# Kernel tuning notes

Hardware: AMD Instinct MI355X
Metric: run time of the kernel (lower is better)

## Reference

```python
import jax, jax.numpy as jnp
import numpy as np

N = 50000      # nodes
E = 800000     # edges
D_IN = 128
HID = 128
L = 3          # local_layers
EPS = 1e-5     # LayerNorm eps


def setup_inputs() -> dict:
    key = jax.random.key(0)
    ks = jax.random.split(key, 8)
    s_in = 1.0 / np.sqrt(D_IN)
    s_h = 1.0 / np.sqrt(HID)
    return {
        "x": jax.random.normal(ks[0], (N, D_IN), jnp.float32),
        "edge_index": jax.random.randint(ks[1], (2, E), 0, N, dtype=jnp.int64),
        "lin_in_w": jax.random.normal(ks[2], (D_IN, HID), jnp.float32) * s_in,
        "lin_in_b": jnp.zeros((HID,), jnp.float32),
        "conv_w": jax.random.normal(ks[3], (L, HID, HID), jnp.float32) * s_h,
        "conv_b": jnp.zeros((L, HID), jnp.float32),
        "lin_w": jax.random.normal(ks[4], (L, HID, HID), jnp.float32) * s_h,
        "lin_b": jnp.zeros((L, HID), jnp.float32),
        "ln_g": jnp.ones((L, HID), jnp.float32),
        "ln_b": jnp.zeros((L, HID), jnp.float32),
    }


def reference(x, edge_index, lin_in_w, lin_in_b, conv_w, conv_b, lin_w, lin_b, ln_g, ln_b):
    # GCNConv(normalize=True, add_self_loops=True): augment with self loops
    loops = jnp.arange(N, dtype=edge_index.dtype)
    src = jnp.concatenate([edge_index[0], loops])
    dst = jnp.concatenate([edge_index[1], loops])
    deg = jax.ops.segment_sum(jnp.ones_like(dst, x.dtype), dst, num_segments=N)
    dinv = jnp.where(deg > 0, jax.lax.rsqrt(deg), 0.0)
    norm = dinv[src] * dinv[dst]  # [E+N]

    # pre_linear (dropout p=0, eval)
    x = x @ lin_in_w + lin_in_b

    x_final = jnp.zeros((N, HID), x.dtype)
    for i in range(L):
        h = x @ conv_w[i]
        agg = jax.ops.segment_sum(h[src] * norm[:, None], dst, num_segments=N) + conv_b[i]
        # residual linear
        x = agg + x @ lin_w[i] + lin_b[i]
        # LayerNorm
        mu = jnp.mean(x, axis=-1, keepdims=True)
        var = jnp.var(x, axis=-1, keepdims=True)
        x = (x - mu) * jax.lax.rsqrt(var + EPS) * ln_g[i] + ln_b[i]
        x = jax.nn.relu(x)
        x_final = x_final + x  # JK sum
    return x_final
```

## Files before the change

kernel.cpp:

```cpp
#include <hip/hip_runtime.h>

#define HID 128
#define LN_EPS 1e-5f

typedef __attribute__((ext_vector_type(8))) short bf16x8;
typedef __attribute__((ext_vector_type(4))) float f32x4;

__device__ __forceinline__ ushort f2bf(float v) {
  union { float f; uint u; } x; x.f = v;
  uint r = x.u + 0x7fffu + ((x.u >> 16) & 1u);
  return (ushort)(r >> 16);
}
__device__ __forceinline__ float bf2f(ushort u) {
  union { uint u; float f; } x; x.u = (uint)u << 16; return x.f;
}


__global__ void k_init(int* __restrict__ cnt, int n) {
  int i = blockIdx.x * 256 + threadIdx.x;
  if (i < n) cnt[i] = 0;
}

__global__ void k_count(const int* __restrict__ dst, int* __restrict__ cnt,
                        int* __restrict__ rank, int E) {
  int e = blockIdx.x * 256 + threadIdx.x;
  if (e < E) rank[e] = atomicAdd(&cnt[dst[e]], 1);
}

__global__ void k_dinv(const int* __restrict__ cnt, float* __restrict__ dinv, int n) {
  int i = blockIdx.x * 256 + threadIdx.x;
  if (i < n) dinv[i] = rsqrtf((float)cnt[i] + 1.0f);
}

__global__ void k_bsum(const int* __restrict__ cnt, int* __restrict__ bsum, int n) {
  __shared__ int red[256];
  int b = blockIdx.x, t = threadIdx.x;
  int i = b * 512 + t * 2;
  int s = ((i < n) ? cnt[i] : 0) + ((i + 1 < n) ? cnt[i + 1] : 0);
  red[t] = s;
  __syncthreads();
  for (int off = 128; off > 0; off >>= 1) {
    if (t < off) red[t] += red[t + off];
    __syncthreads();
  }
  if (t == 0) bsum[b] = red[0];
}

__global__ void k_bscan(int* __restrict__ bsum, int nb) {
  __shared__ int buf[1024];
  int t = threadIdx.x;
  int v = (t < nb) ? bsum[t] : 0;
  buf[t] = v;
  __syncthreads();
  for (int off = 1; off < 1024; off <<= 1) {
    int u = (t >= off) ? buf[t - off] : 0;
    __syncthreads();
    buf[t] += u;
    __syncthreads();
  }
  if (t < nb) bsum[t] = buf[t] - v;
}

__global__ void k_rowstart(const int* __restrict__ cnt, const int* __restrict__ bsum,
                           int* __restrict__ row_start, int n) {
  __shared__ int buf[256];
  int b = blockIdx.x, t = threadIdx.x;
  int i = b * 512 + t * 2;
  int c0 = (i < n) ? cnt[i] : 0;
  int c1 = (i + 1 < n) ? cnt[i + 1] : 0;
  int s = c0 + c1;
  buf[t] = s;
  __syncthreads();
  int mine = s;
  for (int off = 1; off < 256; off <<= 1) {
    int u = (t >= off) ? buf[t - off] : 0;
    __syncthreads();
    buf[t] += u;
    __syncthreads();
  }
  int ex = buf[t] - mine + bsum[b];
  if (i < n) row_start[i] = ex;
  if (i + 1 < n) row_start[i + 1] = ex + c0;
}

__global__ void k_scatter(const int* __restrict__ src, const int* __restrict__ dst,
                          const int* __restrict__ row_start, const int* __restrict__ rank,
                          const float* __restrict__ dinv,
                          uint2* __restrict__ rec, int E) {
  int e = blockIdx.x * 256 + threadIdx.x;
  if (e < E) {
    int d = dst[e], s = src[e];
    int pos = row_start[d] + rank[e];
    union { float f; uint u; } w; w.f = dinv[s] * dinv[d];
    rec[pos] = make_uint2((uint)s, w.u);
  }
}

__global__ void k_prep_w(const float* __restrict__ lin_in_w,
                         const float* __restrict__ conv_w, const float* __restrict__ lin_w,
                         const float* __restrict__ conv_b, const float* __restrict__ lin_b,
                         ushort* __restrict__ wt_in, ushort* __restrict__ wt_l,
                         float* __restrict__ bsum, int L) {
  int tid = blockIdx.x * 256 + threadIdx.x;
  int total = L * 128 * 256;
  if (tid < total) {
    int l = tid >> 15;
    int idx = tid & 32767;
    int n = idx >> 12;
    int r = idx & 4095;
    int ks = r >> 9;
    int r2 = r & 511;
    int lane = r2 >> 3;
    int j = r2 & 7;
    int k2 = ks * 32 + (lane >> 4) * 8 + j;
    int c = n * 16 + (lane & 15);
    float v = (k2 < 128) ? conv_w[((size_t)l * 128 + k2) * 128 + c]
                         : lin_w[((size_t)l * 128 + (k2 - 128)) * 128 + c];
    wt_l[tid] = f2bf(v);
  }
  if (tid < 128 * 128) {
    int n = tid >> 11;
    int r = tid & 2047;
    int ks = r >> 9;
    int r2 = r & 511;
    int lane = r2 >> 3;
    int j = r2 & 7;
    int k = ks * 32 + (lane >> 4) * 8 + j;
    int c = n * 16 + (lane & 15);
    wt_in[tid] = f2bf(lin_in_w[k * 128 + c]);
  }
  if (tid < L * 128) bsum[tid] = conv_b[tid] + lin_b[tid];
}

__global__ void k_agg(const ushort* __restrict__ X, const int* __restrict__ row_start,
                      const int* __restrict__ cnt, const float* __restrict__ dinv,
                      const uint2* __restrict__ rec, ushort* __restrict__ Sout, int n) {
  int node = blockIdx.x * 4 + (threadIdx.x >> 6);
  if (node >= n) return;
  int lane = threadIdx.x & 63;
  float dv = dinv[node];
  uint v = *reinterpret_cast<const uint*>(X + (size_t)node * HID + lane * 2);
  float ax = dv * dv * bf2f((ushort)(v & 0xffff));
  float ay = dv * dv * bf2f((ushort)(v >> 16));
  int start = row_start[node];
  int m = cnt[node];
  int last = start + m - 1;
  const ulong* recq = reinterpret_cast<const ulong*>(rec);

  for (int e = 0; e < m; e += 8) {
    int i0 = start + e;
    ulong q[8];
#pragma unroll
    for (int j = 0; j < 8; j++) q[j] = recq[min(i0 + j, last)];
    uint u[8];
#pragma unroll
    for (int j = 0; j < 8; j++)
      u[j] = *reinterpret_cast<const uint*>(X + (size_t)(uint)q[j] * HID + lane * 2);
#pragma unroll
    for (int j = 0; j < 8; j++) {
      union { uint u; float f; } w;
      w.u = (e + j < m) ? (uint)(q[j] >> 32) : 0u;
      ax = fmaf(w.f, bf2f((ushort)(u[j] & 0xffff)), ax);
      ay = fmaf(w.f, bf2f((ushort)(u[j] >> 16)), ay);
    }
  }
  uint o = (uint)f2bf(ax) | ((uint)f2bf(ay) << 16);
  *reinterpret_cast<uint*>(Sout + (size_t)node * HID + lane * 2) = o;
}


__global__ void __launch_bounds__(256, 2)
k_gemm_in(const float* __restrict__ Xin, const ushort* __restrict__ WtF,
          const float* __restrict__ bias, ushort* __restrict__ Xout, int nrows) {
  __shared__ float lds[4 * 16 * 132];
  const int tid = threadIdx.x;
  const int wid = tid >> 6, lane = tid & 63;
  const int lr = lane & 15, lg = lane >> 4;
  const int r0 = blockIdx.x * 64 + wid * 16;
  const int arow = r0 + lr;
  const bool rowok = arow < nrows;

  bf16x8 a[4];
  {
    const float* xp = Xin + (size_t)arow * HID + lg * 8;
#pragma unroll
    for (int ks = 0; ks < 4; ks++) {
      bf16x8 t;
#pragma unroll
      for (int i = 0; i < 8; i++) t[i] = 0;
      if (rowok) {
        float4 u0 = *reinterpret_cast<const float4*>(xp + ks * 32);
        float4 u1 = *reinterpret_cast<const float4*>(xp + ks * 32 + 4);
        t[0] = (short)f2bf(u0.x); t[1] = (short)f2bf(u0.y);
        t[2] = (short)f2bf(u0.z); t[3] = (short)f2bf(u0.w);
        t[4] = (short)f2bf(u1.x); t[5] = (short)f2bf(u1.y);
        t[6] = (short)f2bf(u1.z); t[7] = (short)f2bf(u1.w);
      }
      a[ks] = t;
    }
  }

  f32x4 acc[8];
#pragma unroll
  for (int n = 0; n < 8; n++) acc[n] = f32x4{0.f, 0.f, 0.f, 0.f};

  const ushort* wb = WtF + lane * 8;
#pragma unroll
  for (int n = 0; n < 8; n++)
#pragma unroll
    for (int ks = 0; ks < 4; ks++) {
      bf16x8 b = *reinterpret_cast<const bf16x8*>(wb + (n * 4 + ks) * 512);
      acc[n] = __builtin_amdgcn_mfma_f32_16x16x32_bf16(a[ks], b, acc[n], 0, 0, 0);
    }

  float* T = lds + wid * (16 * 132);
#pragma unroll
  for (int n = 0; n < 8; n++)
#pragma unroll
    for (int q = 0; q < 4; q++)
      T[(lg * 4 + q) * 132 + n * 16 + lr] = acc[n][q];

  const int c0 = lg * 32;
  const float* Trow = T + lr * 132 + c0;
  const int orow = r0 + lr;
  if (orow < nrows) {
    ushort* xo = Xout + (size_t)orow * HID + c0;
    uint pk[16];
#pragma unroll
    for (int j = 0; j < 8; j++) {
      float4 t = *reinterpret_cast<const float4*>(Trow + j * 4);
      float4 b4 = *reinterpret_cast<const float4*>(bias + c0 + j * 4);
      float o0 = t.x + b4.x, o1 = t.y + b4.y, o2 = t.z + b4.z, o3 = t.w + b4.w;
      pk[j * 2 + 0] = (uint)f2bf(o0) | ((uint)f2bf(o1) << 16);
      pk[j * 2 + 1] = (uint)f2bf(o2) | ((uint)f2bf(o3) << 16);
    }
#pragma unroll
    for (int j = 0; j < 4; j++)
      *reinterpret_cast<uint4*>(xo + j * 8) =
          make_uint4(pk[j * 4 + 0], pk[j * 4 + 1], pk[j * 4 + 2], pk[j * 4 + 3]);
  }
}

__global__ void __launch_bounds__(256, 2)
k_layer(const ushort* __restrict__ S, const ushort* __restrict__ Xin,
        ushort* __restrict__ Xout,
        const ushort* __restrict__ WtF, const float* __restrict__ bsum,
        const float* __restrict__ gamma, const float* __restrict__ beta, int nrows) {
  __shared__ float lds[4 * 16 * 132];
  const int tid = threadIdx.x;
  const int wid = tid >> 6, lane = tid & 63;
  const int lr = lane & 15, lg = lane >> 4;
  const int r0 = blockIdx.x * 64 + wid * 16;
  const int arow = r0 + lr;
  const bool rowok = arow < nrows;

  bf16x8 a[8];
  {
    const ushort* sp = S + (size_t)arow * HID + lg * 8;
    const ushort* xp = Xin + (size_t)arow * HID + lg * 8;
    bf16x8 z;
#pragma unroll
    for (int i = 0; i < 8; i++) z[i] = 0;
#pragma unroll
    for (int ks = 0; ks < 4; ks++)
      a[ks] = rowok ? *reinterpret_cast<const bf16x8*>(sp + ks * 32) : z;
#pragma unroll
    for (int ks = 0; ks < 4; ks++)
      a[4 + ks] = rowok ? *reinterpret_cast<const bf16x8*>(xp + ks * 32) : z;
  }

  f32x4 acc[8];
#pragma unroll
  for (int n = 0; n < 8; n++) acc[n] = f32x4{0.f, 0.f, 0.f, 0.f};

  const ushort* wb = WtF + lane * 8;
#pragma unroll
  for (int n = 0; n < 8; n++)
#pragma unroll
    for (int ks = 0; ks < 8; ks++) {
      bf16x8 b = *reinterpret_cast<const bf16x8*>(wb + (n * 8 + ks) * 512);
      acc[n] = __builtin_amdgcn_mfma_f32_16x16x32_bf16(a[ks], b, acc[n], 0, 0, 0);
    }

  float* T = lds + wid * (16 * 132);
#pragma unroll
  for (int n = 0; n < 8; n++)
#pragma unroll
    for (int q = 0; q < 4; q++)
      T[(lg * 4 + q) * 132 + n * 16 + lr] = acc[n][q];

  const int c0 = lg * 32;
  const float* Trow = T + lr * 132 + c0;
  float v[32];
  float sum = 0.f, sq = 0.f;
#pragma unroll
  for (int j = 0; j < 8; j++) {
    float4 t = *reinterpret_cast<const float4*>(Trow + j * 4);
    float4 b4 = *reinterpret_cast<const float4*>(bsum + c0 + j * 4);
    float x0 = t.x + b4.x, x1 = t.y + b4.y, x2 = t.z + b4.z, x3 = t.w + b4.w;
    v[j * 4 + 0] = x0; v[j * 4 + 1] = x1; v[j * 4 + 2] = x2; v[j * 4 + 3] = x3;
    sum += (x0 + x1) + (x2 + x3);
    sq = fmaf(x0, x0, sq); sq = fmaf(x1, x1, sq);
    sq = fmaf(x2, x2, sq); sq = fmaf(x3, x3, sq);
  }
  sum += __shfl_xor(sum, 16); sq += __shfl_xor(sq, 16);
  sum += __shfl_xor(sum, 32); sq += __shfl_xor(sq, 32);
  const float mean = sum * (1.f / 128.f);
  const float rstd = rsqrtf(sq * (1.f / 128.f) - mean * mean + LN_EPS);

  const int orow = r0 + lr;
  if (orow < nrows) {
    ushort* xo = Xout + (size_t)orow * HID + c0;
    uint pk[16];
#pragma unroll
    for (int j = 0; j < 8; j++) {
      float4 g4 = *reinterpret_cast<const float4*>(gamma + c0 + j * 4);
      float4 b4 = *reinterpret_cast<const float4*>(beta + c0 + j * 4);
      float o0 = fmaxf(fmaf((v[j * 4 + 0] - mean) * rstd, g4.x, b4.x), 0.f);
      float o1 = fmaxf(fmaf((v[j * 4 + 1] - mean) * rstd, g4.y, b4.y), 0.f);
      float o2 = fmaxf(fmaf((v[j * 4 + 2] - mean) * rstd, g4.z, b4.z), 0.f);
      float o3 = fmaxf(fmaf((v[j * 4 + 3] - mean) * rstd, g4.w, b4.w), 0.f);
      pk[j * 2 + 0] = (uint)f2bf(o0) | ((uint)f2bf(o1) << 16);
      pk[j * 2 + 1] = (uint)f2bf(o2) | ((uint)f2bf(o3) << 16);
    }
#pragma unroll
    for (int j = 0; j < 4; j++)
      *reinterpret_cast<uint4*>(xo + j * 8) =
          make_uint4(pk[j * 4 + 0], pk[j * 4 + 1], pk[j * 4 + 2], pk[j * 4 + 3]);
  }
}

__global__ void k_jk(const ushort* __restrict__ a, const ushort* __restrict__ b,
                     const ushort* __restrict__ c, float* __restrict__ out, int total8) {
  int i = blockIdx.x * 256 + threadIdx.x;
  if (i >= total8) return;
  uint4 ua = *reinterpret_cast<const uint4*>(a + (size_t)i * 8);
  uint4 ub = *reinterpret_cast<const uint4*>(b + (size_t)i * 8);
  uint4 uc = *reinterpret_cast<const uint4*>(c + (size_t)i * 8);
  float o[8];
  const uint pa[4] = {ua.x, ua.y, ua.z, ua.w};
  const uint pb[4] = {ub.x, ub.y, ub.z, ub.w};
  const uint pc[4] = {uc.x, uc.y, uc.z, uc.w};
#pragma unroll
  for (int j = 0; j < 4; j++) {
    o[j * 2 + 0] = bf2f((ushort)(pa[j] & 0xffff)) + bf2f((ushort)(pb[j] & 0xffff)) +
                   bf2f((ushort)(pc[j] & 0xffff));
    o[j * 2 + 1] = bf2f((ushort)(pa[j] >> 16)) + bf2f((ushort)(pb[j] >> 16)) +
                   bf2f((ushort)(pc[j] >> 16));
  }
  float* op = out + (size_t)i * 8;
  *reinterpret_cast<float4*>(op) = make_float4(o[0], o[1], o[2], o[3]);
  *reinterpret_cast<float4*>(op + 4) = make_float4(o[4], o[5], o[6], o[7]);
}


extern "C" void kernel_launch(void* const* d_in, const int* in_sizes, int n_in,
                              void* d_out, int out_size, void* d_ws, size_t ws_size,
                              hipStream_t stream) {
  const float* x_in     = (const float*)d_in[0];
  const int*   edge     = (const int*)d_in[1];
  const float* lin_in_w = (const float*)d_in[2];
  const float* lin_in_b = (const float*)d_in[3];
  const float* conv_w   = (const float*)d_in[4];
  const float* conv_b   = (const float*)d_in[5];
  const float* lin_w    = (const float*)d_in[6];
  const float* lin_b    = (const float*)d_in[7];
  const float* ln_g     = (const float*)d_in[8];
  const float* ln_b     = (const float*)d_in[9];

  int N = in_sizes[0] / HID;
  int E = in_sizes[1] / 2;
  int L = in_sizes[4] / (HID * HID);

  const int* src = edge;
  const int* dst = edge + E;

  char* ws = (char*)d_ws;
  size_t off = 0;
  auto alloc = [&](size_t bytes) -> void* {
    void* p = (void*)(ws + off);
    off += (bytes + 255) & ~(size_t)255;
    return p;
  };
  int*    cnt       = (int*)alloc((size_t)N * 4);
  int*    rank      = (int*)alloc((size_t)E * 4);
  int*    row_start = (int*)alloc((size_t)N * 4);
  float*  dinv      = (float*)alloc((size_t)N * 4);
  int*    blocksum  = (int*)alloc(4096);
  uint2*  rec       = (uint2*)alloc((size_t)E * 8);
  ushort* xb0       = (ushort*)alloc((size_t)N * HID * 2);
  ushort* xb1       = (ushort*)alloc((size_t)N * HID * 2);
  ushort* xb2       = (ushort*)alloc((size_t)N * HID * 2);
  ushort* sbuf      = (ushort*)alloc((size_t)N * HID * 2);
  ushort* wt_in     = (ushort*)alloc((size_t)128 * 128 * 2);
  ushort* wt_l      = (ushort*)alloc((size_t)L * 128 * 256 * 2);
  float*  bsum      = (float*)alloc((size_t)L * 128 * 4);
  (void)ws_size; (void)n_in; (void)out_size;

  int nb_n = (N + 255) / 256;
  int nb_e = (E + 255) / 256;
  int nbs  = (N + 511) / 512;
  int nb_g = (N + 63) / 64;
  int nb_w = (L * 128 * 256 + 255) / 256;
  int total8 = N * HID / 8;
  int nb_j = (total8 + 255) / 256;

  k_init<<<nb_n, 256, 0, stream>>>(cnt, N);
  k_count<<<nb_e, 256, 0, stream>>>(dst, cnt, rank, E);
  k_dinv<<<nb_n, 256, 0, stream>>>(cnt, dinv, N);
  k_bsum<<<nbs, 256, 0, stream>>>(cnt, blocksum, N);
  k_bscan<<<1, 1024, 0, stream>>>(blocksum, nbs);
  k_rowstart<<<nbs, 256, 0, stream>>>(cnt, blocksum, row_start, N);
  k_scatter<<<nb_e, 256, 0, stream>>>(src, dst, row_start, rank, dinv, rec, E);
  k_prep_w<<<nb_w, 256, 0, stream>>>(lin_in_w, conv_w, lin_w, conv_b, lin_b,
                                     wt_in, wt_l, bsum, L);

  k_gemm_in<<<nb_g, 256, 0, stream>>>(x_in, wt_in, lin_in_b, xb0, N);

  ushort* xin_b[3]  = {xb0, xb1, xb2};
  ushort* xout_b[3] = {xb1, xb2, xb0};
  for (int i = 0; i < L; i++) {
    k_agg<<<(N + 3) / 4, 256, 0, stream>>>(xin_b[i], row_start, cnt, dinv, rec, sbuf, N);
    k_layer<<<nb_g, 256, 0, stream>>>(sbuf, xin_b[i], xout_b[i],
        wt_l + (size_t)i * 128 * 256, bsum + (size_t)i * 128,
        ln_g + (size_t)i * HID, ln_b + (size_t)i * HID, N);
  }
  k_jk<<<nb_j, 256, 0, stream>>>(xb1, xb2, xb0, (float*)d_out, total8);
}
```

Baseline: 361.2 us.

## Split aggregation into column halves, stage weights in LDS, fuse JK sum and dinv

The dinv computation moves into the block-sum kernel, and the JK summation moves into the last layer kernel. Both changes remove a separate launch, and the JK fusion also skips one full write and read of a bf16 buffer. The aggregation kernel now runs in two passes over 64-column halves, with each wave handling two edges at once and combining them through a cross-lane shuffle. This aims to improve gather locality and cache reuse of node rows, at the cost of reading the edge records twice. The layer GEMM now stages weight tiles through LDS with double-buffered prefetch instead of loading per-lane from global memory, which adds syncs and LDS use that may reduce occupancy.

```diff
diff --git a/kernel.cpp b/kernel.cpp
--- a/kernel.cpp
+++ b/kernel.cpp
@@ -27,17 +27,16 @@
   if (e < E) rank[e] = atomicAdd(&cnt[dst[e]], 1);
 }
 
-__global__ void k_dinv(const int* __restrict__ cnt, float* __restrict__ dinv, int n) {
-  int i = blockIdx.x * 256 + threadIdx.x;
-  if (i < n) dinv[i] = rsqrtf((float)cnt[i] + 1.0f);
-}
-
-__global__ void k_bsum(const int* __restrict__ cnt, int* __restrict__ bsum, int n) {
+__global__ void k_bsum(const int* __restrict__ cnt, int* __restrict__ bsum,
+                       float* __restrict__ dinv, int n) {
   __shared__ int red[256];
   int b = blockIdx.x, t = threadIdx.x;
   int i = b * 512 + t * 2;
-  int s = ((i < n) ? cnt[i] : 0) + ((i + 1 < n) ? cnt[i + 1] : 0);
-  red[t] = s;
+  int c0 = (i < n) ? cnt[i] : 0;
+  int c1 = (i + 1 < n) ? cnt[i + 1] : 0;
+  if (i < n) dinv[i] = rsqrtf((float)c0 + 1.0f);
+  if (i + 1 < n) dinv[i + 1] = rsqrtf((float)c1 + 1.0f);
+  red[t] = c0 + c1;
   __syncthreads();
   for (int off = 128; off > 0; off >>= 1) {
     if (t < off) red[t] += red[t + off];
@@ -134,38 +133,48 @@
 
 __global__ void k_agg(const ushort* __restrict__ X, const int* __restrict__ row_start,
                       const int* __restrict__ cnt, const float* __restrict__ dinv,
-                      const uint2* __restrict__ rec, ushort* __restrict__ Sout, int n) {
+                      const uint2* __restrict__ rec, ushort* __restrict__ Sout,
+                      int n, int colh) {
   int node = blockIdx.x * 4 + (threadIdx.x >> 6);
   if (node >= n) return;
-  int lane = threadIdx.x & 63;
-  float dv = dinv[node];
-  uint v = *reinterpret_cast<const uint*>(X + (size_t)node * HID + lane * 2);
-  float ax = dv * dv * bf2f((ushort)(v & 0xffff));
-  float ay = dv * dv * bf2f((ushort)(v >> 16));
-  int start = row_start[node];
-  int m = cnt[node];
-  int last = start + m - 1;
+  const int lane = threadIdx.x & 63;
+  const int e2 = lane >> 5;
+  const int cg = lane & 31;
+  const int colb = colh * 64 + cg * 2;
+
+  float ax = 0.f, ay = 0.f;
+  const int start = row_start[node];
+  const int m = cnt[node];
+  const int last = start + m - 1;
   const ulong* recq = reinterpret_cast<const ulong*>(rec);
 
-  for (int e = 0; e < m; e += 8) {
-    int i0 = start + e;
+  for (int e = 0; e < m; e += 16) {
     ulong q[8];
 #pragma unroll
-    for (int j = 0; j < 8; j++) q[j] = recq[min(i0 + j, last)];
+    for (int j = 0; j < 8; j++) q[j] = recq[min(start + e + 2 * j + e2, last)];
     uint u[8];
 #pragma unroll
     for (int j = 0; j < 8; j++)
-      u[j] = *reinterpret_cast<const uint*>(X + (size_t)(uint)q[j] * HID + lane * 2);
+      u[j] = *reinterpret_cast<const uint*>(X + (size_t)(uint)q[j] * HID + colb);
 #pragma unroll
     for (int j = 0; j < 8; j++) {
       union { uint u; float f; } w;
-      w.u = (e + j < m) ? (uint)(q[j] >> 32) : 0u;
+      w.u = (e + 2 * j + e2 < m) ? (uint)(q[j] >> 32) : 0u;
       ax = fmaf(w.f, bf2f((ushort)(u[j] & 0xffff)), ax);
       ay = fmaf(w.f, bf2f((ushort)(u[j] >> 16)), ay);
     }
   }
-  uint o = (uint)f2bf(ax) | ((uint)f2bf(ay) << 16);
-  *reinterpret_cast<uint*>(Sout + (size_t)node * HID + lane * 2) = o;
+  ax += __shfl_xor(ax, 32);
+  ay += __shfl_xor(ay, 32);
+  if (e2 == 0) {
+    float dv = dinv[node];
+    float d2 = dv * dv;
+    uint v = *reinterpret_cast<const uint*>(X + (size_t)node * HID + colb);
+    ax = fmaf(d2, bf2f((ushort)(v & 0xffff)), ax);
+    ay = fmaf(d2, bf2f((ushort)(v >> 16)), ay);
+    *reinterpret_cast<uint*>(Sout + (size_t)node * HID + colb) =
+        (uint)f2bf(ax) | ((uint)f2bf(ay) << 16);
+  }
 }
 
 
@@ -245,7 +254,10 @@
 k_layer(const ushort* __restrict__ S, const ushort* __restrict__ Xin,
         ushort* __restrict__ Xout,
         const ushort* __restrict__ WtF, const float* __restrict__ bsum,
-        const float* __restrict__ gamma, const float* __restrict__ beta, int nrows) {
+        const float* __restrict__ gamma, const float* __restrict__ beta, int nrows,
+        int last, const ushort* __restrict__ jk1, const ushort* __restrict__ jk2,
+        float* __restrict__ out) {
+  __shared__ ushort wlds[8192];
   __shared__ float lds[4 * 16 * 132];
   const int tid = threadIdx.x;
   const int wid = tid >> 6, lane = tid & 63;
@@ -273,14 +285,32 @@
 #pragma unroll
   for (int n = 0; n < 8; n++) acc[n] = f32x4{0.f, 0.f, 0.f, 0.f};
 
-  const ushort* wb = WtF + lane * 8;
-#pragma unroll
-  for (int n = 0; n < 8; n++)
-#pragma unroll
-    for (int ks = 0; ks < 8; ks++) {
-      bf16x8 b = *reinterpret_cast<const bf16x8*>(wb + (n * 8 + ks) * 512);
-      acc[n] = __builtin_amdgcn_mfma_f32_16x16x32_bf16(a[ks], b, acc[n], 0, 0, 0);
-    }
+  const uint4* gW = reinterpret_cast<const uint4*>(WtF);
+  uint4* ldsW = reinterpret_cast<uint4*>(wlds);
+  uint4 stg[4];
+#pragma unroll
+  for (int p = 0; p < 4; p++) stg[p] = gW[p * 256 + tid];
+#pragma unroll
+  for (int np = 0; np < 4; np++) {
+#pragma unroll
+    for (int p = 0; p < 4; p++) ldsW[p * 256 + tid] = stg[p];
+    __syncthreads();
+    if (np < 3) {
+#pragma unroll
+      for (int p = 0; p < 4; p++) stg[p] = gW[(np + 1) * 1024 + p * 256 + tid];
+    }
+#pragma unroll
+    for (int nn = 0; nn < 2; nn++) {
+      const int n = np * 2 + nn;
+      const ushort* wb2 = wlds + nn * 8 * 512 + lane * 8;
+#pragma unroll
+      for (int ks = 0; ks < 8; ks++) {
+        bf16x8 b = *reinterpret_cast<const bf16x8*>(wb2 + ks * 512);
+        acc[n] = __builtin_amdgcn_mfma_f32_16x16x32_bf16(a[ks], b, acc[n], 0, 0, 0);
+      }
+    }
+    __syncthreads();
+  }
 
   float* T = lds + wid * (16 * 132);
 #pragma unroll
@@ -310,47 +340,49 @@
 
   const int orow = r0 + lr;
   if (orow < nrows) {
-    ushort* xo = Xout + (size_t)orow * HID + c0;
-    uint pk[16];
+    float o[32];
 #pragma unroll
     for (int j = 0; j < 8; j++) {
       float4 g4 = *reinterpret_cast<const float4*>(gamma + c0 + j * 4);
       float4 b4 = *reinterpret_cast<const float4*>(beta + c0 + j * 4);
-      float o0 = fmaxf(fmaf((v[j * 4 + 0] - mean) * rstd, g4.x, b4.x), 0.f);
-      float o1 = fmaxf(fmaf((v[j * 4 + 1] - mean) * rstd, g4.y, b4.y), 0.f);
-      float o2 = fmaxf(fmaf((v[j * 4 + 2] - mean) * rstd, g4.z, b4.z), 0.f);
-      float o3 = fmaxf(fmaf((v[j * 4 + 3] - mean) * rstd, g4.w, b4.w), 0.f);
-      pk[j * 2 + 0] = (uint)f2bf(o0) | ((uint)f2bf(o1) << 16);
-      pk[j * 2 + 1] = (uint)f2bf(o2) | ((uint)f2bf(o3) << 16);
-    }
-#pragma unroll
-    for (int j = 0; j < 4; j++)
-      *reinterpret_cast<uint4*>(xo + j * 8) =
-          make_uint4(pk[j * 4 + 0], pk[j * 4 + 1], pk[j * 4 + 2], pk[j * 4 + 3]);
-  }
-}
-
-__global__ void k_jk(const ushort* __restrict__ a, const ushort* __restrict__ b,
-                     const ushort* __restrict__ c, float* __restrict__ out, int total8) {
-  int i = blockIdx.x * 256 + threadIdx.x;
-  if (i >= total8) return;
-  uint4 ua = *reinterpret_cast<const uint4*>(a + (size_t)i * 8);
-  uint4 ub = *reinterpret_cast<const uint4*>(b + (size_t)i * 8);
-  uint4 uc = *reinterpret_cast<const uint4*>(c + (size_t)i * 8);
-  float o[8];
-  const uint pa[4] = {ua.x, ua.y, ua.z, ua.w};
-  const uint pb[4] = {ub.x, ub.y, ub.z, ub.w};
-  const uint pc[4] = {uc.x, uc.y, uc.z, uc.w};
-#pragma unroll
-  for (int j = 0; j < 4; j++) {
-    o[j * 2 + 0] = bf2f((ushort)(pa[j] & 0xffff)) + bf2f((ushort)(pb[j] & 0xffff)) +
-                   bf2f((ushort)(pc[j] & 0xffff));
-    o[j * 2 + 1] = bf2f((ushort)(pa[j] >> 16)) + bf2f((ushort)(pb[j] >> 16)) +
-                   bf2f((ushort)(pc[j] >> 16));
-  }
-  float* op = out + (size_t)i * 8;
-  *reinterpret_cast<float4*>(op) = make_float4(o[0], o[1], o[2], o[3]);
-  *reinterpret_cast<float4*>(op + 4) = make_float4(o[4], o[5], o[6], o[7]);
+      o[j * 4 + 0] = fmaxf(fmaf((v[j * 4 + 0] - mean) * rstd, g4.x, b4.x), 0.f);
+      o[j * 4 + 1] = fmaxf(fmaf((v[j * 4 + 1] - mean) * rstd, g4.y, b4.y), 0.f);
+      o[j * 4 + 2] = fmaxf(fmaf((v[j * 4 + 2] - mean) * rstd, g4.z, b4.z), 0.f);
+      o[j * 4 + 3] = fmaxf(fmaf((v[j * 4 + 3] - mean) * rstd, g4.w, b4.w), 0.f);
+    }
+    if (!last) {
+      ushort* xo = Xout + (size_t)orow * HID + c0;
+      uint pk[16];
+#pragma unroll
+      for (int j = 0; j < 16; j++)
+        pk[j] = (uint)f2bf(o[j * 2]) | ((uint)f2bf(o[j * 2 + 1]) << 16);
+#pragma unroll
+      for (int j = 0; j < 4; j++)
+        *reinterpret_cast<uint4*>(xo + j * 8) =
+            make_uint4(pk[j * 4 + 0], pk[j * 4 + 1], pk[j * 4 + 2], pk[j * 4 + 3]);
+    } else {
+      const ushort* p1 = jk1 + (size_t)orow * HID + c0;
+      const ushort* p2 = jk2 + (size_t)orow * HID + c0;
+      float* op = out + (size_t)orow * HID + c0;
+#pragma unroll
+      for (int j = 0; j < 4; j++) {
+        uint4 u1 = *reinterpret_cast<const uint4*>(p1 + j * 8);
+        uint4 u2 = *reinterpret_cast<const uint4*>(p2 + j * 8);
+        const uint w1[4] = {u1.x, u1.y, u1.z, u1.w};
+        const uint w2[4] = {u2.x, u2.y, u2.z, u2.w};
+        float r[8];
+#pragma unroll
+        for (int q = 0; q < 4; q++) {
+          r[q * 2 + 0] = o[j * 8 + q * 2 + 0] +
+                         bf2f((ushort)(w1[q] & 0xffff)) + bf2f((ushort)(w2[q] & 0xffff));
+          r[q * 2 + 1] = o[j * 8 + q * 2 + 1] +
+                         bf2f((ushort)(w1[q] >> 16)) + bf2f((ushort)(w2[q] >> 16));
+        }
+        *reinterpret_cast<float4*>(op + j * 8) = make_float4(r[0], r[1], r[2], r[3]);
+        *reinterpret_cast<float4*>(op + j * 8 + 4) = make_float4(r[4], r[5], r[6], r[7]);
+      }
+    }
+  }
 }
 
 
@@ -402,13 +434,11 @@
   int nbs  = (N + 511) / 512;
   int nb_g = (N + 63) / 64;
   int nb_w = (L * 128 * 256 + 255) / 256;
-  int total8 = N * HID / 8;
-  int nb_j = (total8 + 255) / 256;
+  int nb_a = (N + 3) / 4;
 
   k_init<<<nb_n, 256, 0, stream>>>(cnt, N);
   k_count<<<nb_e, 256, 0, stream>>>(dst, cnt, rank, E);
-  k_dinv<<<nb_n, 256, 0, stream>>>(cnt, dinv, N);
-  k_bsum<<<nbs, 256, 0, stream>>>(cnt, blocksum, N);
+  k_bsum<<<nbs, 256, 0, stream>>>(cnt, blocksum, dinv, N);
   k_bscan<<<1, 1024, 0, stream>>>(blocksum, nbs);
   k_rowstart<<<nbs, 256, 0, stream>>>(cnt, blocksum, row_start, N);
   k_scatter<<<nb_e, 256, 0, stream>>>(src, dst, row_start, rank, dinv, rec, E);
@@ -420,10 +450,12 @@
   ushort* xin_b[3]  = {xb0, xb1, xb2};
   ushort* xout_b[3] = {xb1, xb2, xb0};
   for (int i = 0; i < L; i++) {
-    k_agg<<<(N + 3) / 4, 256, 0, stream>>>(xin_b[i], row_start, cnt, dinv, rec, sbuf, N);
+    k_agg<<<nb_a, 256, 0, stream>>>(xin_b[i], row_start, cnt, dinv, rec, sbuf, N, 0);
+    k_agg<<<nb_a, 256, 0, stream>>>(xin_b[i], row_start, cnt, dinv, rec, sbuf, N, 1);
+    int last = (i == L - 1) ? 1 : 0;
     k_layer<<<nb_g, 256, 0, stream>>>(sbuf, xin_b[i], xout_b[i],
         wt_l + (size_t)i * 128 * 256, bsum + (size_t)i * 128,
-        ln_g + (size_t)i * HID, ln_b + (size_t)i * HID, N);
-  }
-  k_jk<<<nb_j, 256, 0, stream>>>(xb1, xb2, xb0, (float*)d_out, total8);
-}
+        ln_g + (size_t)i * HID, ln_b + (size_t)i * HID, N,
+        last, xb1, xb2, (float*)d_out);
+  }
+}
```

After: 424.2 us. 17.5% more time.
